# Optimization experiments

Measured on AMD Instinct MI355X. Metric: run time of the kernel, lower is better.

## Reference

```python
import jax, jax.numpy as jnp
import numpy as np

K = 6  # kernel size (square)
_LP = (K - 1) // 2          # 2: PyTorch 'same' left pad for even kernel
_RP = (K - 1) - _LP         # 3: right pad


@jax.custom_vjp
def spike_boxcar(x):
    # Heaviside step with boxcar surrogate gradient (DECOLLE-style)
    return (x > 0).astype(x.dtype)

def _spike_fwd(x):
    return spike_boxcar(x), x

def _spike_bwd(x, g):
    # grad is passed through only where -0.5 < x <= 0.5
    return (jnp.where((x > -0.5) & (x <= 0.5), g, jnp.zeros_like(g)),)

spike_boxcar.defvjp(_spike_fwd, _spike_bwd)


def setup_inputs() -> dict:
    key = jax.random.key(0)
    kx, kw = jax.random.split(key)
    B, Cin, H, W, T = 32, 1, 64, 64, 100
    Cout = 8
    x = jax.random.normal(kx, (B, Cin, H, W, T), dtype=jnp.float32)
    # Conv2d default init: U(-1/sqrt(fan_in), 1/sqrt(fan_in)), fan_in = Cin*K*K
    bound = 1.0 / np.sqrt(Cin * K * K)
    w = jax.random.uniform(kw, (Cout, Cin, K, K), dtype=jnp.float32,
                           minval=-bound, maxval=bound)
    thresh = jnp.full((1,), 0.8, dtype=jnp.float32)
    return {"x": x, "w": w, "thresh": thresh}


def reference(x, w, thresh):
    B, Cin, H, W, T = x.shape
    Cout = w.shape[0]
    # Batch all timesteps into one conv call (conv is independent of state)
    xt = jnp.moveaxis(x, -1, 0).reshape(T * B, Cin, H, W)
    Wx = jax.lax.conv_general_dilated(
        xt, w, window_strides=(1, 1),
        padding=[(_LP, _RP), (_LP, _RP)],
        dimension_numbers=("NCHW", "OIHW", "NCHW"),
    ).reshape(T, B, Cout, H, W)

    ut0 = jnp.zeros((B, Cout, H, W), dtype=x.dtype)
    st0 = jnp.zeros_like(ut0)

    def step(carry, wx):
        ut, st = carry
        ut = ut - st * thresh[0] + wx
        st = spike_boxcar(ut)
        return (ut, st), st

    _, s = jax.lax.scan(step, (ut0, st0), Wx)  # s: [T, B, Cout, H, W]
    return jnp.moveaxis(s, 0, -1)              # [B, Cout, H, W, T]
```

## Files before the change

### kernel.cpp

```cpp
#include <hip/hip_runtime.h>

#define HH 64
#define WW 64
#define TT 100
#define CO 8
#define COB 4
#define KS 6
#define LP 2
#define HALO 21
#define NSITE 441
#define NG 5

__device__ __forceinline__ float stepu(float u, float s, float th, float wx) {
    return __fadd_rn(__fsub_rn(u, __fmul_rn(s, th)), wx);
}

template<int T0>
__device__ __forceinline__ void process_chunk(
    const float* __restrict__ xb,
    float4* __restrict__ xs, const float (*wds)[COB],
    int tid, int r, int c, int h0, int w0, float th,
    float* ut, float* sprev, unsigned* bw )
{
    for (int i = tid; i < NSITE * NG; i += 256) {
        const int s  = i / NG;
        const int tg = i - s * NG;
        const int hr = s / HALO;
        const int hc = s - hr * HALO;
        const int hh = h0 - LP + hr;
        const int ww = w0 - LP + hc;
        float4 v = make_float4(0.f, 0.f, 0.f, 0.f);
        if ((unsigned)hh < (unsigned)HH && (unsigned)ww < (unsigned)WW)
            v = *(const float4*)(xb + ((size_t)hh * WW + ww) * TT + T0 + tg * 4);
        xs[tg * NSITE + s] = v;
    }
    __syncthreads();

    unsigned cb[COB];
#pragma unroll
    for (int j = 0; j < COB; ++j) cb[j] = 0u;

    for (int tg = 0; tg < NG; ++tg) {
        float4 wx[COB];
#pragma unroll
        for (int j = 0; j < COB; ++j) wx[j] = make_float4(0.f, 0.f, 0.f, 0.f);
#pragma unroll
        for (int kh = 0; kh < KS; ++kh) {
#pragma unroll
            for (int kw = 0; kw < KS; ++kw) {
                const float4 xv = xs[tg * NSITE + (r + kh) * HALO + (c + kw)];
                const int tap = kh * KS + kw;
#pragma unroll
                for (int j = 0; j < COB; ++j) {
                    const float wd = wds[tap][j];
                    wx[j].x = __fmaf_rn(wd, xv.x, wx[j].x);
                    wx[j].y = __fmaf_rn(wd, xv.y, wx[j].y);
                    wx[j].z = __fmaf_rn(wd, xv.z, wx[j].z);
                    wx[j].w = __fmaf_rn(wd, xv.w, wx[j].w);
                }
            }
        }
        const int sh = tg * 4;
#pragma unroll
        for (int j = 0; j < COB; ++j) {
            float u = ut[j], s = sprev[j];
            unsigned m = 0u;
            u = stepu(u, s, th, wx[j].x); s = (u > 0.f) ? 1.f : 0.f; m |= (u > 0.f) ? 1u : 0u;
            u = stepu(u, s, th, wx[j].y); s = (u > 0.f) ? 1.f : 0.f; m |= (u > 0.f) ? 2u : 0u;
            u = stepu(u, s, th, wx[j].z); s = (u > 0.f) ? 1.f : 0.f; m |= (u > 0.f) ? 4u : 0u;
            u = stepu(u, s, th, wx[j].w); s = (u > 0.f) ? 1.f : 0.f; m |= (u > 0.f) ? 8u : 0u;
            ut[j] = u; sprev[j] = s;
            cb[j] |= m << sh;
        }
    }
    __syncthreads();

    constexpr int W0 = T0 / 32;
    constexpr int S  = T0 % 32;
#pragma unroll
    for (int j = 0; j < COB; ++j) {
        bw[j * 4 + W0] |= cb[j] << S;
        if constexpr (S + 20 > 32)
            bw[j * 4 + W0 + 1] |= cb[j] >> ((32 - S) & 31);
    }
}

__global__ __launch_bounds__(256, 2)
void sconv2d_spike_kernel(const float* __restrict__ x,
                          const float* __restrict__ wgt,
                          const float* __restrict__ thresh,
                          float* __restrict__ out)
{
    __shared__ float4   xs[NG * NSITE];
    __shared__ float    wds[KS * KS][COB];
    __shared__ unsigned stg[4][256];

    const int tid = threadIdx.x;

    const int blk  = blockIdx.x;
    const int b    = blk >> 5;
    const int rest = blk & 31;
    const int tb   = rest >> 1;
    const int co0  = (rest & 1) * COB;
    const int h0   = (tb >> 2) << 4;
    const int w0   = (tb & 3) << 4;
    const int r    = tid >> 4;
    const int c    = tid & 15;

    for (int i = tid; i < KS * KS * COB; i += 256) {
        const int j   = i / (KS * KS);
        const int tap = i - j * (KS * KS);
        wds[tap][j] = wgt[(co0 + j) * (KS * KS) + tap];
    }
    const float th = thresh[0];

    const float* xb   = x   + (size_t)b * (HH * WW * TT);
    float*       outb = out + (size_t)b * (CO * HH * WW * TT);

    float ut[COB], sprev[COB];
    unsigned bw[COB * 4];
#pragma unroll
    for (int j = 0; j < COB; ++j) { ut[j] = 0.f; sprev[j] = 0.f; }
#pragma unroll
    for (int i = 0; i < COB * 4; ++i) bw[i] = 0u;

    process_chunk< 0>(xb, xs, wds, tid, r, c, h0, w0, th, ut, sprev, bw);
    process_chunk<20>(xb, xs, wds, tid, r, c, h0, w0, th, ut, sprev, bw);
    process_chunk<40>(xb, xs, wds, tid, r, c, h0, w0, th, ut, sprev, bw);
    process_chunk<60>(xb, xs, wds, tid, r, c, h0, w0, th, ut, sprev, bw);
    process_chunk<80>(xb, xs, wds, tid, r, c, h0, w0, th, ut, sprev, bw);

#pragma unroll
    for (int j = 0; j < COB; ++j) {
        const int co = co0 + j;
        stg[0][tid] = bw[j * 4 + 0];
        stg[1][tid] = bw[j * 4 + 1];
        stg[2][tid] = bw[j * 4 + 2];
        stg[3][tid] = bw[j * 4 + 3];
        __syncthreads();
#pragma unroll
        for (int k = 0; k < 25; ++k) {
            const int idx = tid + k * 256;
            const int u   = idx / 25;
            const int tt  = (idx - u * 25) * 4;
            const unsigned bs = stg[tt >> 5][u] >> (tt & 31);
            float4 v;
            v.x = (float)( bs        & 1u);
            v.y = (float)((bs >> 1)  & 1u);
            v.z = (float)((bs >> 2)  & 1u);
            v.w = (float)((bs >> 3)  & 1u);
            const int rr = u >> 4, cc = u & 15;
            *(float4*)(outb + (((size_t)co * HH + (h0 + rr)) * WW + (w0 + cc)) * TT + tt) = v;
        }
        __syncthreads();
    }
}

extern "C" void kernel_launch(void* const* d_in, const int* in_sizes, int n_in,
                              void* d_out, int out_size, void* d_ws, size_t ws_size,
                              hipStream_t stream) {
    const float* x      = (const float*)d_in[0];
    const float* wgt    = (const float*)d_in[1];
    const float* thresh = (const float*)d_in[2];
    float* out = (float*)d_out;

    dim3 grid(32 * 16 * 2);
    dim3 block(256);
    sconv2d_spike_kernel<<<grid, block, 0, stream>>>(x, wgt, thresh, out);
}
```

Measured before the change: 561.5 us.

## Split spike kernel into compute and bit-expand kernels via workspace

Splits the fused kernel in two. The first runs the convolution and spike recurrence and writes packed spike bits to a workspace. The second reads those bits and expands them to float outputs at higher occupancy. The intent is to keep the heavy output-store phase from holding the compute kernel's large shared-memory footprint, so stores run with more resident blocks. The cost is an extra launch plus a workspace write and read of 16 MB, and the original fused kernel remains as a fallback when the workspace is too small.

```diff
diff --git a/kernel.cpp b/kernel.cpp
--- a/kernel.cpp
+++ b/kernel.cpp
@@ -85,27 +85,32 @@
     }
 }
 
-__global__ __launch_bounds__(256, 2)
-void sconv2d_spike_kernel(const float* __restrict__ x,
-                          const float* __restrict__ wgt,
-                          const float* __restrict__ thresh,
-                          float* __restrict__ out)
-{
-    __shared__ float4   xs[NG * NSITE];
-    __shared__ float    wds[KS * KS][COB];
-    __shared__ unsigned stg[4][256];
-
-    const int tid = threadIdx.x;
-
-    const int blk  = blockIdx.x;
-    const int b    = blk >> 5;
+__device__ __forceinline__ void block_geom(int blk, int tid,
+                                           int& b, int& co0, int& h0, int& w0,
+                                           int& r, int& c) {
+    b    = blk >> 5;
     const int rest = blk & 31;
     const int tb   = rest >> 1;
-    const int co0  = (rest & 1) * COB;
-    const int h0   = (tb >> 2) << 4;
-    const int w0   = (tb & 3) << 4;
-    const int r    = tid >> 4;
-    const int c    = tid & 15;
+    co0  = (rest & 1) * COB;
+    h0   = (tb >> 2) << 4;
+    w0   = (tb & 3) << 4;
+    r    = tid >> 4;
+    c    = tid & 15;
+}
+
+__global__ __launch_bounds__(256, 2)
+void sconv_compute(const float* __restrict__ x,
+                   const float* __restrict__ wgt,
+                   const float* __restrict__ thresh,
+                   uint4* __restrict__ bits_ws)
+{
+    __shared__ float4 xs[NG * NSITE];
+    __shared__ float  wds[KS * KS][COB];
+
+    const int tid = threadIdx.x;
+    const int blk = blockIdx.x;
+    int b, co0, h0, w0, r, c;
+    block_geom(blk, tid, b, co0, h0, w0, r, c);
 
     for (int i = tid; i < KS * KS * COB; i += 256) {
         const int j   = i / (KS * KS);
@@ -114,8 +119,7 @@
     }
     const float th = thresh[0];
 
-    const float* xb   = x   + (size_t)b * (HH * WW * TT);
-    float*       outb = out + (size_t)b * (CO * HH * WW * TT);
+    const float* xb = x + (size_t)b * (HH * WW * TT);
 
     float ut[COB], sprev[COB];
     unsigned bw[COB * 4];
@@ -131,12 +135,33 @@
     process_chunk<80>(xb, xs, wds, tid, r, c, h0, w0, th, ut, sprev, bw);
 
 #pragma unroll
+    for (int j = 0; j < COB; ++j)
+        bits_ws[((size_t)blk * COB + j) * 256 + tid] =
+            make_uint4(bw[j * 4 + 0], bw[j * 4 + 1], bw[j * 4 + 2], bw[j * 4 + 3]);
+}
+
+__global__ __launch_bounds__(256, 4)
+void sconv_expand(const uint4* __restrict__ bits_ws,
+                  float* __restrict__ out)
+{
+    __shared__ unsigned stg[4][256];
+
+    const int tid = threadIdx.x;
+    const int blk = blockIdx.x;
+    int b, co0, h0, w0, r, c;
+    block_geom(blk, tid, b, co0, h0, w0, r, c);
+    (void)r; (void)c;
+
+    float* outb = out + (size_t)b * (CO * HH * WW * TT);
+
+#pragma unroll
     for (int j = 0; j < COB; ++j) {
         const int co = co0 + j;
-        stg[0][tid] = bw[j * 4 + 0];
-        stg[1][tid] = bw[j * 4 + 1];
-        stg[2][tid] = bw[j * 4 + 2];
-        stg[3][tid] = bw[j * 4 + 3];
+        const uint4 bv = bits_ws[((size_t)blk * COB + j) * 256 + tid];
+        stg[0][tid] = bv.x;
+        stg[1][tid] = bv.y;
+        stg[2][tid] = bv.z;
+        stg[3][tid] = bv.w;
         __syncthreads();
 #pragma unroll
         for (int k = 0; k < 25; ++k) {
@@ -156,6 +181,70 @@
     }
 }
 
+__global__ __launch_bounds__(256, 2)
+void sconv2d_spike_mono(const float* __restrict__ x,
+                        const float* __restrict__ wgt,
+                        const float* __restrict__ thresh,
+                        float* __restrict__ out)
+{
+    __shared__ float4   xs[NG * NSITE];
+    __shared__ float    wds[KS * KS][COB];
+    __shared__ unsigned stg[4][256];
+
+    const int tid = threadIdx.x;
+    const int blk = blockIdx.x;
+    int b, co0, h0, w0, r, c;
+    block_geom(blk, tid, b, co0, h0, w0, r, c);
+
+    for (int i = tid; i < KS * KS * COB; i += 256) {
+        const int j   = i / (KS * KS);
+        const int tap = i - j * (KS * KS);
+        wds[tap][j] = wgt[(co0 + j) * (KS * KS) + tap];
+    }
+    const float th = thresh[0];
+
+    const float* xb   = x   + (size_t)b * (HH * WW * TT);
+    float*       outb = out + (size_t)b * (CO * HH * WW * TT);
+
+    float ut[COB], sprev[COB];
+    unsigned bw[COB * 4];
+#pragma unroll
+    for (int j = 0; j < COB; ++j) { ut[j] = 0.f; sprev[j] = 0.f; }
+#pragma unroll
+    for (int i = 0; i < COB * 4; ++i) bw[i] = 0u;
+
+    process_chunk< 0>(xb, xs, wds, tid, r, c, h0, w0, th, ut, sprev, bw);
+    process_chunk<20>(xb, xs, wds, tid, r, c, h0, w0, th, ut, sprev, bw);
+    process_chunk<40>(xb, xs, wds, tid, r, c, h0, w0, th, ut, sprev, bw);
+    process_chunk<60>(xb, xs, wds, tid, r, c, h0, w0, th, ut, sprev, bw);
+    process_chunk<80>(xb, xs, wds, tid, r, c, h0, w0, th, ut, sprev, bw);
+
+#pragma unroll
+    for (int j = 0; j < COB; ++j) {
+        const int co = co0 + j;
+        stg[0][tid] = bw[j * 4 + 0];
+        stg[1][tid] = bw[j * 4 + 1];
+        stg[2][tid] = bw[j * 4 + 2];
+        stg[3][tid] = bw[j * 4 + 3];
+        __syncthreads();
+#pragma unroll
+        for (int k = 0; k < 25; ++k) {
+            const int idx = tid + k * 256;
+            const int u   = idx / 25;
+            const int tt  = (idx - u * 25) * 4;
+            const unsigned bs = stg[tt >> 5][u] >> (tt & 31);
+            float4 v;
+            v.x = (float)( bs        & 1u);
+            v.y = (float)((bs >> 1)  & 1u);
+            v.z = (float)((bs >> 2)  & 1u);
+            v.w = (float)((bs >> 3)  & 1u);
+            const int rr = u >> 4, cc = u & 15;
+            *(float4*)(outb + (((size_t)co * HH + (h0 + rr)) * WW + (w0 + cc)) * TT + tt) = v;
+        }
+        __syncthreads();
+    }
+}
+
 extern "C" void kernel_launch(void* const* d_in, const int* in_sizes, int n_in,
                               void* d_out, int out_size, void* d_ws, size_t ws_size,
                               hipStream_t stream) {
@@ -164,7 +253,15 @@
     const float* thresh = (const float*)d_in[2];
     float* out = (float*)d_out;
 
+    const size_t need = (size_t)1024 * COB * 256 * sizeof(uint4);
     dim3 grid(32 * 16 * 2);
     dim3 block(256);
-    sconv2d_spike_kernel<<<grid, block, 0, stream>>>(x, wgt, thresh, out);
-}
+
+    if (ws_size >= need) {
+        uint4* bits_ws = (uint4*)d_ws;
+        sconv_compute<<<grid, block, 0, stream>>>(x, wgt, thresh, bits_ws);
+        sconv_expand <<<grid, block, 0, stream>>>(bits_ws, out);
+    } else {
+        sconv2d_spike_mono<<<grid, block, 0, stream>>>(x, wgt, thresh, out);
+    }
+}
```

After: 646.8 us. 1.15x slower.

## Compute all eight output channels per block to reuse staged input tile

Applied to the files above, without the earlier changes.

Each block now computes all 8 output channels instead of 4, halving the grid. The goal is to stop loading and staging the same input halo twice per spatial tile. Spike bitmasks move from per-thread registers into a shared-memory array, which removes the per-channel syncs in the write-out. In exchange it raises register pressure (8 float4 accumulators), grows LDS use, and leaves only 512 blocks, which may underfill the GPU and reduce latency hiding.

```diff
diff --git a/kernel.cpp b/kernel.cpp
--- a/kernel.cpp
+++ b/kernel.cpp
@@ -4,7 +4,6 @@
 #define WW 64
 #define TT 100
 #define CO 8
-#define COB 4
 #define KS 6
 #define LP 2
 #define HALO 21
@@ -18,9 +17,10 @@
 template<int T0>
 __device__ __forceinline__ void process_chunk(
     const float* __restrict__ xb,
-    float4* __restrict__ xs, const float (*wds)[COB],
+    float4* __restrict__ xs, const float (*wds)[CO],
+    unsigned (*bwl)[4][256],
     int tid, int r, int c, int h0, int w0, float th,
-    float* ut, float* sprev, unsigned* bw )
+    float* ut, float* sprev)
 {
     for (int i = tid; i < NSITE * NG; i += 256) {
         const int s  = i / NG;
@@ -36,14 +36,14 @@
     }
     __syncthreads();
 
-    unsigned cb[COB];
+    unsigned cb[CO];
 #pragma unroll
-    for (int j = 0; j < COB; ++j) cb[j] = 0u;
+    for (int j = 0; j < CO; ++j) cb[j] = 0u;
 
     for (int tg = 0; tg < NG; ++tg) {
-        float4 wx[COB];
+        float4 wx[CO];
 #pragma unroll
-        for (int j = 0; j < COB; ++j) wx[j] = make_float4(0.f, 0.f, 0.f, 0.f);
+        for (int j = 0; j < CO; ++j) wx[j] = make_float4(0.f, 0.f, 0.f, 0.f);
 #pragma unroll
         for (int kh = 0; kh < KS; ++kh) {
 #pragma unroll
@@ -51,7 +51,7 @@
                 const float4 xv = xs[tg * NSITE + (r + kh) * HALO + (c + kw)];
                 const int tap = kh * KS + kw;
 #pragma unroll
-                for (int j = 0; j < COB; ++j) {
+                for (int j = 0; j < CO; ++j) {
                     const float wd = wds[tap][j];
                     wx[j].x = __fmaf_rn(wd, xv.x, wx[j].x);
                     wx[j].y = __fmaf_rn(wd, xv.y, wx[j].y);
@@ -62,7 +62,7 @@
         }
         const int sh = tg * 4;
 #pragma unroll
-        for (int j = 0; j < COB; ++j) {
+        for (int j = 0; j < CO; ++j) {
             float u = ut[j], s = sprev[j];
             unsigned m = 0u;
             u = stepu(u, s, th, wx[j].x); s = (u > 0.f) ? 1.f : 0.f; m |= (u > 0.f) ? 1u : 0u;
@@ -78,10 +78,10 @@
     constexpr int W0 = T0 / 32;
     constexpr int S  = T0 % 32;
 #pragma unroll
-    for (int j = 0; j < COB; ++j) {
-        bw[j * 4 + W0] |= cb[j] << S;
+    for (int j = 0; j < CO; ++j) {
+        bwl[j][W0][tid] |= cb[j] << S;
         if constexpr (S + 20 > 32)
-            bw[j * 4 + W0 + 1] |= cb[j] >> ((32 - S) & 31);
+            bwl[j][W0 + 1][tid] |= cb[j] >> ((32 - S) & 31);
     }
 }
 
@@ -92,67 +92,62 @@
                           float* __restrict__ out)
 {
     __shared__ float4   xs[NG * NSITE];
-    __shared__ float    wds[KS * KS][COB];
-    __shared__ unsigned stg[4][256];
+    __shared__ float    wds[KS * KS][CO];
+    __shared__ unsigned bwl[CO][4][256];
 
     const int tid = threadIdx.x;
 
-    const int blk  = blockIdx.x;
-    const int b    = blk >> 5;
-    const int rest = blk & 31;
-    const int tb   = rest >> 1;
-    const int co0  = (rest & 1) * COB;
-    const int h0   = (tb >> 2) << 4;
-    const int w0   = (tb & 3) << 4;
-    const int r    = tid >> 4;
-    const int c    = tid & 15;
+    const int blk = blockIdx.x;
+    const int b   = blk >> 4;
+    const int tb  = blk & 15;
+    const int h0  = (tb >> 2) << 4;
+    const int w0  = (tb & 3) << 4;
+    const int r   = tid >> 4;
+    const int c   = tid & 15;
 
-    for (int i = tid; i < KS * KS * COB; i += 256) {
+    for (int i = tid; i < KS * KS * CO; i += 256) {
         const int j   = i / (KS * KS);
         const int tap = i - j * (KS * KS);
-        wds[tap][j] = wgt[(co0 + j) * (KS * KS) + tap];
+        wds[tap][j] = wgt[j * (KS * KS) + tap];
+    }
+#pragma unroll
+    for (int j = 0; j < CO; ++j) {
+        bwl[j][0][tid] = 0u; bwl[j][1][tid] = 0u;
+        bwl[j][2][tid] = 0u; bwl[j][3][tid] = 0u;
     }
     const float th = thresh[0];
 
     const float* xb   = x   + (size_t)b * (HH * WW * TT);
     float*       outb = out + (size_t)b * (CO * HH * WW * TT);
 
-    float ut[COB], sprev[COB];
-    unsigned bw[COB * 4];
+    float ut[CO], sprev[CO];
 #pragma unroll
-    for (int j = 0; j < COB; ++j) { ut[j] = 0.f; sprev[j] = 0.f; }
-#pragma unroll
-    for (int i = 0; i < COB * 4; ++i) bw[i] = 0u;
+    for (int j = 0; j < CO; ++j) { ut[j] = 0.f; sprev[j] = 0.f; }
 
-    process_chunk< 0>(xb, xs, wds, tid, r, c, h0, w0, th, ut, sprev, bw);
-    process_chunk<20>(xb, xs, wds, tid, r, c, h0, w0, th, ut, sprev, bw);
-    process_chunk<40>(xb, xs, wds, tid, r, c, h0, w0, th, ut, sprev, bw);
-    process_chunk<60>(xb, xs, wds, tid, r, c, h0, w0, th, ut, sprev, bw);
-    process_chunk<80>(xb, xs, wds, tid, r, c, h0, w0, th, ut, sprev, bw);
+    process_chunk< 0>(xb, xs, wds, bwl, tid, r, c, h0, w0, th, ut, sprev);
+    process_chunk<20>(xb, xs, wds, bwl, tid, r, c, h0, w0, th, ut, sprev);
+    process_chunk<40>(xb, xs, wds, bwl, tid, r, c, h0, w0, th, ut, sprev);
+    process_chunk<60>(xb, xs, wds, bwl, tid, r, c, h0, w0, th, ut, sprev);
+    process_chunk<80>(xb, xs, wds, bwl, tid, r, c, h0, w0, th, ut, sprev);
+
+    __syncthreads();
 
 #pragma unroll
-    for (int j = 0; j < COB; ++j) {
-        const int co = co0 + j;
-        stg[0][tid] = bw[j * 4 + 0];
-        stg[1][tid] = bw[j * 4 + 1];
-        stg[2][tid] = bw[j * 4 + 2];
-        stg[3][tid] = bw[j * 4 + 3];
-        __syncthreads();
+    for (int j = 0; j < CO; ++j) {
 #pragma unroll
         for (int k = 0; k < 25; ++k) {
             const int idx = tid + k * 256;
             const int u   = idx / 25;
             const int tt  = (idx - u * 25) * 4;
-            const unsigned bs = stg[tt >> 5][u] >> (tt & 31);
+            const unsigned bs = bwl[j][tt >> 5][u] >> (tt & 31);
             float4 v;
             v.x = (float)( bs        & 1u);
             v.y = (float)((bs >> 1)  & 1u);
             v.z = (float)((bs >> 2)  & 1u);
             v.w = (float)((bs >> 3)  & 1u);
             const int rr = u >> 4, cc = u & 15;
-            *(float4*)(outb + (((size_t)co * HH + (h0 + rr)) * WW + (w0 + cc)) * TT + tt) = v;
+            *(float4*)(outb + (((size_t)j * HH + (h0 + rr)) * WW + (w0 + cc)) * TT + tt) = v;
         }
-        __syncthreads();
     }
 }
 
@@ -164,7 +159,7 @@
     const float* thresh = (const float*)d_in[2];
     float* out = (float*)d_out;
 
-    dim3 grid(32 * 16 * 2);
+    dim3 grid(32 * 16);
     dim3 block(256);
     sconv2d_spike_kernel<<<grid, block, 0, stream>>>(x, wgt, thresh, out);
 }
```

Result: slower. 1.323 ms (+135.7%).
